# Performance work log

Hardware: AMD Instinct MI355X
Metric: run time of the kernel (lower is better)

## Reference

```python
import jax, jax.numpy as jnp
import numpy as np

NUM_HEADS = 8
CHANNELS = 512


def setup_inputs() -> dict:
    key = jax.random.key(0)
    k1, k2, k3, k4, k5 = jax.random.split(key, 5)
    C = CHANNELS
    x = jax.random.normal(k1, (8, C, 64, 64), dtype=jnp.float32)
    # 1x1 conv weights stored as (out_ch, in_ch) matrices
    qkv_w = jax.random.normal(k2, (3 * C, C), dtype=jnp.float32) * (C ** -0.5)
    qkv_b = jax.random.normal(k3, (3 * C,), dtype=jnp.float32) * 0.02
    proj_w = jax.random.normal(k4, (C, C), dtype=jnp.float32) * (C ** -0.5)
    proj_b = jax.random.normal(k5, (C,), dtype=jnp.float32) * 0.02
    return {"x": x, "qkv_w": qkv_w, "qkv_b": qkv_b, "proj_w": proj_w, "proj_b": proj_b}


def reference(x, qkv_w, qkv_b, proj_w, proj_b):
    B, C, H, W = x.shape
    heads = NUM_HEADS
    d = C // heads
    N = H * W
    scale = d ** -0.5
    # 1x1 conv == per-pixel matmul over channels
    qkv = jnp.einsum('bchw,oc->bohw', x, qkv_w) + qkv_b[None, :, None, None]
    qkv = qkv.reshape(B, 3, heads, d, N)
    q, k, v = qkv[:, 0], qkv[:, 1], qkv[:, 2]  # each (B, heads, d, N)
    # NOTE: attention over the channel dim -> (B, heads, d, d), as in the torch code
    attn = jax.nn.softmax(jnp.einsum('bhdn,bhen->bhde', q, k) * scale, axis=-1)
    # dropout is identity in eval mode
    out = jnp.einsum('bhde,bhen->bhdn', attn, v).reshape(B, C, H, W)
    out = jnp.einsum('bchw,oc->bohw', out, proj_w) + proj_b[None, :, None, None]
    return out, attn.mean(axis=1)  # (B,C,H,W), (B,d,d)
```

## Files before the change

kernel.cpp:

```cpp
#include <hip/hip_runtime.h>
#include <cstdio>
#include <cstdint>

#define BATCH 8
#define CH    512
#define OC3   1536
#define QKROWS 1024
#define NPIX  4096
#define HEADS 8
#define HDIM  64
#define KDEPTH 512
#define SCALE 0.125f
#define NSPLIT 8

typedef __bf16 bf16;
typedef __bf16 bf16x4 __attribute__((ext_vector_type(4)));
typedef __bf16 bf16x8 __attribute__((ext_vector_type(8)));
typedef float  f32x4  __attribute__((ext_vector_type(4)));

#define AS1 __attribute__((address_space(1)))
#define AS3 __attribute__((address_space(3)))

__global__ __launch_bounds__(256) void convert_bf16_kernel(
    const float* __restrict__ in, bf16* __restrict__ out, int n)
{
    const int i = blockIdx.x * 256 + threadIdx.x;
    if (i < n) out[i] = (bf16)in[i];
}

__global__ __launch_bounds__(256) void wvt_kernel(
    const bf16* __restrict__ wv, bf16* __restrict__ wvt)
{
    const int c0 = blockIdx.x * 64;
    const int d0 = blockIdx.y * 64;
    __shared__ bf16 tl[64][72];
    const int t = threadIdx.x;

    #pragma unroll
    for (int i = 0; i < 2; ++i) {
        const int lin = t + 256 * i;
        const int row = lin >> 3;
        const int c8  = (lin & 7) * 8;
        *(bf16x8*)&tl[row][c8] = *(const bf16x8*)(wv + (size_t)(d0 + row) * CH + c0 + c8);
    }
    __syncthreads();
    #pragma unroll
    for (int i = 0; i < 2; ++i) {
        const int lin  = t + 256 * i;
        const int crow = lin >> 3;
        const int d8   = (lin & 7) * 8;
        bf16x8 v;
        #pragma unroll
        for (int j = 0; j < 8; ++j) v[j] = tl[d8 + j][crow];
        *(bf16x8*)(wvt + (size_t)(c0 + crow) * CH + d0 + d8) = v;
    }
}

__global__ __launch_bounds__(256) void transpose_convert_kernel(
    const float* __restrict__ src, bf16* __restrict__ dst)
{
    const int b  = blockIdx.z;
    const int n0 = blockIdx.x * 64;
    const int c0 = blockIdx.y * 64;
    __shared__ float tile[64][65];
    const int t = threadIdx.x;
    const float* xp = src + (size_t)b * CH * NPIX;

    #pragma unroll
    for (int i = 0; i < 4; ++i) {
        const int lin = t + 256 * i;
        const int r   = lin >> 4;
        const int c4  = (lin & 15) * 4;
        const float4 v = *(const float4*)(xp + (size_t)(c0 + r) * 4096 + n0 + c4);
        tile[r][c4 + 0] = v.x; tile[r][c4 + 1] = v.y;
        tile[r][c4 + 2] = v.z; tile[r][c4 + 3] = v.w;
    }
    __syncthreads();

    bf16* op = dst + (size_t)b * NPIX * CH;
    #pragma unroll
    for (int i = 0; i < 2; ++i) {
        const int lin = t + 256 * i;
        const int n   = lin >> 3;
        const int c8  = (lin & 7) * 8;
        bf16x8 v;
        #pragma unroll
        for (int jj = 0; jj < 8; ++jj) v[jj] = (bf16)tile[c8 + jj][n];
        *(bf16x8*)(op + (size_t)(n0 + n) * CH + c0 + c8) = v;
    }
}

__global__ __launch_bounds__(256) void gemm_qk_kernel(
    const bf16* __restrict__ A, const bf16* __restrict__ Bt,
    const float* __restrict__ bias, bf16* __restrict__ qkb)
{
    const int nwg  = gridDim.x * gridDim.y;
    const int orig = blockIdx.x + gridDim.x * blockIdx.y;
    const int wg   = (orig & 7) * (nwg >> 3) + (orig >> 3);
    const int by   = wg % gridDim.y;
    const int bx   = wg / gridDim.y;

    const int b  = blockIdx.z;
    const int m0 = by * 128;
    const int n0 = bx * 128;
    const bf16* Ap = A;
    const bf16* Bp = Bt + (size_t)b * NPIX * KDEPTH;

    __shared__ bf16 smem[16384];

    const int t    = threadIdx.x;
    const int lane = t & 63;
    const int wave = t >> 6;
    const int wr   = wave >> 1, wc = wave & 1;

    f32x4 acc[4][4];
    const f32x4 zf = {0.f, 0.f, 0.f, 0.f};
    #pragma unroll
    for (int i = 0; i < 4; ++i)
        #pragma unroll
        for (int j = 0; j < 4; ++j) acc[i][j] = zf;

    auto STAGE = [&](int p, int k0) {
        #pragma unroll
        for (int i = 0; i < 2; ++i) {
            const int c   = t + 256 * i;
            const int row = c >> 2;
            const int kb  = ((c & 3) ^ ((row >> 1) & 3)) * 8;
            __builtin_amdgcn_global_load_lds(
                (const AS1 void*)(Ap + (size_t)(m0 + row) * KDEPTH + k0 + kb),
                (AS3 void*)(smem + p * 8192 + c * 8), 16, 0, 0);
            __builtin_amdgcn_global_load_lds(
                (const AS1 void*)(Bp + (size_t)(n0 + row) * KDEPTH + k0 + kb),
                (AS3 void*)(smem + p * 8192 + 4096 + c * 8), 16, 0, 0);
        }
    };

    STAGE(0, 0);
    __syncthreads();
    int cur = 0;

    for (int kt = 0; kt < KDEPTH / 32; ++kt) {
        if (kt < KDEPTH / 32 - 1) STAGE(cur ^ 1, (kt + 1) * 32);

        const bf16* AsP = smem + cur * 8192;
        const bf16* BsP = AsP + 4096;
        bf16x8 af[4], bfv[4];
        #pragma unroll
        for (int i = 0; i < 4; ++i) {
            const int ar = wr * 64 + i * 16 + (lane & 15);
            const int ja = (lane >> 4) ^ ((ar >> 1) & 3);
            af[i]  = *(const bf16x8*)(AsP + ar * 32 + ja * 8);
            const int br = wc * 64 + i * 16 + (lane & 15);
            const int jb = (lane >> 4) ^ ((br >> 1) & 3);
            bfv[i] = *(const bf16x8*)(BsP + br * 32 + jb * 8);
        }
        #pragma unroll
        for (int i = 0; i < 4; ++i)
            #pragma unroll
            for (int j = 0; j < 4; ++j)
                acc[i][j] = __builtin_amdgcn_mfma_f32_16x16x32_bf16(
                    af[i], bfv[j], acc[i][j], 0, 0, 0);

        __syncthreads();
        cur ^= 1;
    }

    {
        bf16* ct = smem;
        #pragma unroll
        for (int i = 0; i < 4; ++i) {
            const int ml = wr * 64 + i * 16 + (lane >> 4) * 4;
            #pragma unroll
            for (int r = 0; r < 4; ++r) {
                const float bv = bias[m0 + ml + r];
                #pragma unroll
                for (int j = 0; j < 4; ++j) {
                    const int n = wc * 64 + j * 16 + (lane & 15);
                    ct[(ml + r) * 128 + n] = (bf16)(acc[i][j][r] + bv);
                }
            }
        }
        __syncthreads();
        bf16* Qp = qkb + (size_t)b * QKROWS * NPIX;
        #pragma unroll
        for (int ii = 0; ii < 8; ++ii) {
            const int c   = t + 256 * ii;
            const int row = c >> 4;
            const int seg = c & 15;
            const int4 v = *(const int4*)(ct + row * 128 + seg * 8);
            *(int4*)(Qp + (size_t)(m0 + row) * NPIX + n0 + seg * 8) = v;
        }
    }
}

__global__ __launch_bounds__(256) void qk_partial_kernel(
    const bf16* __restrict__ qk, float* __restrict__ part)
{
    const int s  = blockIdx.x;
    const int bh = blockIdx.y;
    const int b = bh >> 3, h = bh & 7;
    const bf16* qbase = qk + ((size_t)b * QKROWS + h * HDIM) * NPIX;
    const bf16* kbase = qk + ((size_t)b * QKROWS + CH + h * HDIM) * NPIX;

    __shared__ bf16 smem[16384];

    const int t    = threadIdx.x;
    const int lane = t & 63;
    const int wave = t >> 6;

    f32x4 acc[4];
    const f32x4 zf = {0.f, 0.f, 0.f, 0.f};
    #pragma unroll
    for (int j = 0; j < 4; ++j) acc[j] = zf;

    auto STAGE = [&](int p, int n0) {
        #pragma unroll
        for (int i = 0; i < 2; ++i) {
            const int c   = t + 256 * i;
            const int row = c >> 3;
            const int nb  = ((c & 7) ^ (row & 7)) * 8;
            __builtin_amdgcn_global_load_lds(
                (const AS1 void*)(qbase + (size_t)row * NPIX + n0 + nb),
                (AS3 void*)(smem + p * 8192 + c * 8), 16, 0, 0);
            __builtin_amdgcn_global_load_lds(
                (const AS1 void*)(kbase + (size_t)row * NPIX + n0 + nb),
                (AS3 void*)(smem + p * 8192 + 4096 + c * 8), 16, 0, 0);
        }
    };

    STAGE(0, s * 512);
    __syncthreads();
    int cur = 0;

    for (int nc = 0; nc < 8; ++nc) {
        if (nc < 7) STAGE(cur ^ 1, s * 512 + (nc + 1) * 64);

        const bf16* Qs = smem + cur * 8192;
        const bf16* Ks = Qs + 4096;
        #pragma unroll
        for (int ks = 0; ks < 2; ++ks) {
            const int dr = wave * 16 + (lane & 15);
            const int ja = (ks * 4 + (lane >> 4)) ^ (dr & 7);
            const bf16x8 af = *(const bf16x8*)(Qs + dr * 64 + ja * 8);
            #pragma unroll
            for (int j = 0; j < 4; ++j) {
                const int er = j * 16 + (lane & 15);
                const int jb = (ks * 4 + (lane >> 4)) ^ (er & 7);
                const bf16x8 bf_ = *(const bf16x8*)(Ks + er * 64 + jb * 8);
                acc[j] = __builtin_amdgcn_mfma_f32_16x16x32_bf16(af, bf_, acc[j], 0, 0, 0);
            }
        }
        __syncthreads();
        cur ^= 1;
    }

    float* pb = part + (((size_t)bh * NSPLIT + s) * 64) * 64;
    #pragma unroll
    for (int j = 0; j < 4; ++j)
        #pragma unroll
        for (int r = 0; r < 4; ++r)
            pb[(size_t)(wave * 16 + (lane >> 4) * 4 + r) * 64 + j * 16 + (lane & 15)] = acc[j][r];
}

__global__ __launch_bounds__(256) void qk_reduce_softmax_kernel(
    const float* __restrict__ part, float* __restrict__ attn)
{
    const int bh = blockIdx.x;
    const int t  = threadIdx.x;
    const int r  = t >> 2;
    const int e0 = (t & 3) * 16;

    float v[16];
    #pragma unroll
    for (int i = 0; i < 16; ++i) v[i] = 0.f;

    const float* pb = part + ((size_t)bh * NSPLIT * 64) * 64 + r * 64 + e0;
    for (int s = 0; s < NSPLIT; ++s) {
        const float* ps = pb + (size_t)s * 4096;
        #pragma unroll
        for (int c4 = 0; c4 < 4; ++c4) {
            const float4 p = *(const float4*)(ps + c4 * 4);
            v[c4 * 4 + 0] += p.x; v[c4 * 4 + 1] += p.y;
            v[c4 * 4 + 2] += p.z; v[c4 * 4 + 3] += p.w;
        }
    }

    float m = -1e30f;
    #pragma unroll
    for (int i = 0; i < 16; ++i) m = fmaxf(m, v[i]);
    m = fmaxf(m, __shfl_xor(m, 1));
    m = fmaxf(m, __shfl_xor(m, 2));

    float sum = 0.f;
    #pragma unroll
    for (int i = 0; i < 16; ++i) {
        v[i] = __expf((v[i] - m) * SCALE);
        sum += v[i];
    }
    sum += __shfl_xor(sum, 1);
    sum += __shfl_xor(sum, 2);
    const float inv = 1.f / sum;

    float* arow = attn + ((size_t)bh * 64 + r) * 64 + e0;
    #pragma unroll
    for (int c4 = 0; c4 < 4; ++c4) {
        float4 o;
        o.x = v[c4 * 4 + 0] * inv; o.y = v[c4 * 4 + 1] * inv;
        o.z = v[c4 * 4 + 2] * inv; o.w = v[c4 * 4 + 3] * inv;
        *(float4*)(arow + c4 * 4) = o;
    }
}

__global__ __launch_bounds__(256) void attn_mean_kernel(
    const float* __restrict__ attn, float* __restrict__ om)
{
    const int idx = blockIdx.x * 256 + threadIdx.x;
    const int b = idx >> 12, de = idx & 4095;
    float s = 0.f;
    #pragma unroll
    for (int h = 0; h < 8; ++h)
        s += attn[(((size_t)b * 8 + h) << 12) + de];
    om[idx] = s * 0.125f;
}

__global__ __launch_bounds__(256) void wprime_kernel(
    const float* __restrict__ proj_w, const float* __restrict__ attn,
    bf16* __restrict__ wp)
{
    const int o0 = blockIdx.x * 64;
    const int h  = blockIdx.y;
    const int b  = blockIdx.z;

    __shared__ float ws[64][65];
    __shared__ float as_[64][65];

    const int t = threadIdx.x;
    #pragma unroll
    for (int i = 0; i < 4; ++i) {
        const int lin = t + 256 * i;
        const int r   = lin >> 4;
        const int c4  = (lin & 15) * 4;
        const float4 wv = *(const float4*)(proj_w + (size_t)(o0 + r) * CH + h * HDIM + c4);
        ws[r][c4 + 0] = wv.x; ws[r][c4 + 1] = wv.y;
        ws[r][c4 + 2] = wv.z; ws[r][c4 + 3] = wv.w;
        const float4 av = *(const float4*)(attn + (((size_t)(b * 8 + h) * 64) + r) * 64 + c4);
        as_[r][c4 + 0] = av.x; as_[r][c4 + 1] = av.y;
        as_[r][c4 + 2] = av.z; as_[r][c4 + 3] = av.w;
    }
    __syncthreads();

    const int tx = t & 15, ty = t >> 4;
    const int to = ty * 4, te = tx * 4;
    float acc[4][4] = {};
    for (int d = 0; d < 64; ++d) {
        float a[4], bb[4];
        #pragma unroll
        for (int i = 0; i < 4; ++i) a[i]  = ws[to + i][d];
        #pragma unroll
        for (int j = 0; j < 4; ++j) bb[j] = as_[d][te + j];
        #pragma unroll
        for (int i = 0; i < 4; ++i)
            #pragma unroll
            for (int j = 0; j < 4; ++j)
                acc[i][j] = fmaf(a[i], bb[j], acc[i][j]);
    }

    bf16* wb = wp + (size_t)b * CH * CH;
    #pragma unroll
    for (int i = 0; i < 4; ++i)
        #pragma unroll
        for (int j = 0; j < 4; ++j)
            wb[(size_t)(o0 + to + i) * CH + h * HDIM + te + j] = (bf16)acc[i][j];
}

__global__ __launch_bounds__(256) void bias2_kernel(
    const bf16* __restrict__ wp, const float* __restrict__ bv,
    const float* __restrict__ pb, float* __restrict__ bias2)
{
    const int idx = blockIdx.x * 256 + threadIdx.x;
    const int b = idx >> 9, o = idx & 511;
    const bf16* wr = wp + ((size_t)b * CH + o) * CH;
    float s = 0.f;
    for (int d = 0; d < 512; ++d) s += (float)wr[d] * bv[d];
    bias2[idx] = s + pb[o];
}

__global__ __launch_bounds__(256) void gemm128_kernel(
    const bf16* __restrict__ A, const bf16* __restrict__ Bt,
    const float* __restrict__ bias, size_t bias_bstride,
    float* __restrict__ Cf, bf16* __restrict__ Cb,
    int ncols, int c_rows, size_t a_bstride, size_t bt_bstride)
{
    const int nwg  = gridDim.x * gridDim.y;
    const int orig = blockIdx.x + gridDim.x * blockIdx.y;
    const int wg   = (orig & 7) * (nwg >> 3) + (orig >> 3);
    const int by   = wg % gridDim.y;
    const int bx   = wg / gridDim.y;

    const int b  = blockIdx.z;
    const int m0 = by * 128;
    const int n0 = bx * 128;
    const bf16* Ap = A  + (size_t)b * a_bstride;
    const bf16* Bp = Bt + (size_t)b * bt_bstride;

    __shared__ bf16 smem[16384];

    const int t    = threadIdx.x;
    const int lane = t & 63;
    const int wave = t >> 6;
    const int wr   = wave >> 1, wc = wave & 1;

    f32x4 acc[4][4];
    const f32x4 zf = {0.f, 0.f, 0.f, 0.f};
    #pragma unroll
    for (int i = 0; i < 4; ++i)
        #pragma unroll
        for (int j = 0; j < 4; ++j) acc[i][j] = zf;

    auto STAGE = [&](int p, int k0) {
        #pragma unroll
        for (int i = 0; i < 2; ++i) {
            const int c   = t + 256 * i;
            const int row = c >> 2;
            const int kb  = ((c & 3) ^ ((row >> 1) & 3)) * 8;
            __builtin_amdgcn_global_load_lds(
                (const AS1 void*)(Ap + (size_t)(m0 + row) * KDEPTH + k0 + kb),
                (AS3 void*)(smem + p * 8192 + c * 8), 16, 0, 0);
            __builtin_amdgcn_global_load_lds(
                (const AS1 void*)(Bp + (size_t)(n0 + row) * KDEPTH + k0 + kb),
                (AS3 void*)(smem + p * 8192 + 4096 + c * 8), 16, 0, 0);
        }
    };

    STAGE(0, 0);
    __syncthreads();
    int cur = 0;

    for (int kt = 0; kt < KDEPTH / 32; ++kt) {
        if (kt < KDEPTH / 32 - 1) STAGE(cur ^ 1, (kt + 1) * 32);

        const bf16* AsP = smem + cur * 8192;
        const bf16* BsP = AsP + 4096;
        bf16x8 af[4], bfv[4];
        #pragma unroll
        for (int i = 0; i < 4; ++i) {
            const int ar = wr * 64 + i * 16 + (lane & 15);
            const int ja = (lane >> 4) ^ ((ar >> 1) & 3);
            af[i]  = *(const bf16x8*)(AsP + ar * 32 + ja * 8);
            const int br = wc * 64 + i * 16 + (lane & 15);
            const int jb = (lane >> 4) ^ ((br >> 1) & 3);
            bfv[i] = *(const bf16x8*)(BsP + br * 32 + jb * 8);
        }
        #pragma unroll
        for (int i = 0; i < 4; ++i)
            #pragma unroll
            for (int j = 0; j < 4; ++j)
                acc[i][j] = __builtin_amdgcn_mfma_f32_16x16x32_bf16(
                    af[i], bfv[j], acc[i][j], 0, 0, 0);

        __syncthreads();
        cur ^= 1;
    }

    if (Cb) {
        #pragma unroll
        for (int i = 0; i < 4; ++i) {
            const int mb = m0 + wr * 64 + i * 16 + (lane >> 4) * 4;
            #pragma unroll
            for (int r = 0; r < 4; ++r) {
                const int m  = mb + r;
                const float bv = bias ? bias[b * bias_bstride + m] : 0.f;
                #pragma unroll
                for (int j = 0; j < 4; ++j) {
                    const int n = n0 + wc * 64 + j * 16 + (lane & 15);
                    Cb[(size_t)b * c_rows * ncols + (size_t)m * ncols + n] =
                        (bf16)(acc[i][j][r] + bv);
                }
            }
        }
    } else {
        float* ct = (float*)smem;
        float* Cp = Cf + (size_t)b * c_rows * ncols;
        #pragma unroll
        for (int p = 0; p < 2; ++p) {
            if (wc == p) {
                #pragma unroll
                for (int i = 0; i < 4; ++i) {
                    const int ml = wr * 64 + i * 16 + (lane >> 4) * 4;
                    #pragma unroll
                    for (int r = 0; r < 4; ++r) {
                        const float bv = bias ? bias[b * bias_bstride + m0 + ml + r] : 0.f;
                        #pragma unroll
                        for (int j = 0; j < 4; ++j) {
                            const int n = j * 16 + (lane & 15);
                            ct[(ml + r) * 64 + n] = acc[i][j][r] + bv;
                        }
                    }
                }
            }
            __syncthreads();
            #pragma unroll
            for (int ii = 0; ii < 8; ++ii) {
                const int c   = t + 256 * ii;
                const int row = c >> 4;
                const int seg = c & 15;
                const float4 v = *(const float4*)(ct + row * 64 + seg * 4);
                *(float4*)(Cp + (size_t)(m0 + row) * ncols + n0 + p * 64 + seg * 4) = v;
            }
            __syncthreads();
        }
    }
}

extern "C" void kernel_launch(void* const* d_in, const int* in_sizes, int n_in,
                              void* d_out, int out_size, void* d_ws, size_t ws_size,
                              hipStream_t stream)
{
    (void)in_sizes; (void)n_in; (void)out_size;
    const float* x      = (const float*)d_in[0];
    const float* qkv_w  = (const float*)d_in[1];
    const float* qkv_b  = (const float*)d_in[2];
    const float* proj_w = (const float*)d_in[3];
    const float* proj_b = (const float*)d_in[4];

    float* out       = (float*)d_out;
    float* attn_mean = out + (size_t)BATCH * CH * NPIX;

    const size_t qk_bytes   = (size_t)BATCH * QKROWS * NPIX * 2;
    const size_t xt_bytes   = (size_t)BATCH * NPIX * CH * 2;
    const size_t wq_bytes   = (size_t)OC3 * KDEPTH * 2;
    const size_t attn_bytes = (size_t)BATCH * HEADS * HDIM * HDIM * 4;
    const size_t part_bytes = (size_t)BATCH * HEADS * NSPLIT * HDIM * HDIM * 4;
    const size_t wp_bytes   = (size_t)BATCH * CH * CH * 2;
    const size_t wpp_bytes  = (size_t)BATCH * CH * CH * 2;
    const size_t wvt_bytes  = (size_t)CH * CH * 2;
    const size_t b2_bytes   = (size_t)BATCH * CH * 4;
    const size_t need = qk_bytes + xt_bytes + wq_bytes + attn_bytes + part_bytes +
                        wp_bytes + wpp_bytes + wvt_bytes + b2_bytes;
    if (ws_size < need) {
        fprintf(stderr, "[kernel_launch] ws_size=%zu < need=%zu — abort\n", ws_size, need);
        fflush(stderr);
        return;
    }

    char* p = (char*)d_ws;
    bf16*  qk     = (bf16*)p;             p += qk_bytes;
    bf16*  xt     = (bf16*)p;             p += xt_bytes;
    bf16*  wq_b   = (bf16*)p;             p += wq_bytes;
    float* attn   = (float*)p;            p += attn_bytes;
    float* part   = (float*)p;            p += part_bytes;
    bf16*  wprime = (bf16*)p;             p += wp_bytes;
    bf16*  wpp    = (bf16*)p;             p += wpp_bytes;
    bf16*  wvt    = (bf16*)p;             p += wvt_bytes;
    float* bias2  = (float*)p;

    convert_bf16_kernel<<<dim3((OC3 * KDEPTH + 255) / 256), 256, 0, stream>>>(
        qkv_w, wq_b, OC3 * KDEPTH);
    wvt_kernel<<<dim3(8, 8), 256, 0, stream>>>(wq_b + (size_t)2 * CH * KDEPTH, wvt);

    transpose_convert_kernel<<<dim3(NPIX / 64, CH / 64, BATCH), 256, 0, stream>>>(x, xt);

    gemm_qk_kernel<<<dim3(NPIX / 128, QKROWS / 128, BATCH), 256, 0, stream>>>(
        wq_b, xt, qkv_b, qk);

    qk_partial_kernel<<<dim3(NSPLIT, BATCH * HEADS), 256, 0, stream>>>(qk, part);
    qk_reduce_softmax_kernel<<<dim3(BATCH * HEADS), 256, 0, stream>>>(part, attn);

    attn_mean_kernel<<<dim3(BATCH * HDIM * HDIM / 256), 256, 0, stream>>>(attn, attn_mean);

    wprime_kernel<<<dim3(CH / 64, HEADS, BATCH), 256, 0, stream>>>(proj_w, attn, wprime);

    gemm128_kernel<<<dim3(CH / 128, CH / 128, BATCH), 256, 0, stream>>>(
        wprime, wvt, nullptr, 0, nullptr, wpp, CH, CH, (size_t)CH * CH, 0);
    bias2_kernel<<<dim3(BATCH * CH / 256), 256, 0, stream>>>(
        wprime, qkv_b + 2 * CH, proj_b, bias2);

    gemm128_kernel<<<dim3(NPIX / 128, CH / 128, BATCH), 256, 0, stream>>>(
        wpp, xt, bias2, CH, out, nullptr, NPIX, CH, (size_t)CH * CH,
        (size_t)NPIX * KDEPTH);
}
```

Baseline: 162.4 us.

## Triple-buffer GEMM K-loop with raw barriers and fuse weight convert/transpose

Both 128x128 bf16 GEMM kernels move from a double-buffered LDS pipeline to a three-stage ring. Two tiles stay in flight, and a single s_waitcnt vmcnt(4) plus s_barrier per iteration replaces the full __syncthreads. MFMA blocks are wrapped in s_setprio to favour matrix issue, and the weight fp32->bf16 conversion and V-weight transpose are merged into one launch. This aims to hide global-load latency and cut a launch, at the cost of 50% more LDS per block, which may lower occupancy.

```diff
diff --git a/kernel.cpp b/kernel.cpp
--- a/kernel.cpp
+++ b/kernel.cpp
@@ -21,27 +21,30 @@
 #define AS1 __attribute__((address_space(1)))
 #define AS3 __attribute__((address_space(3)))
 
-__global__ __launch_bounds__(256) void convert_bf16_kernel(
-    const float* __restrict__ in, bf16* __restrict__ out, int n)
-{
-    const int i = blockIdx.x * 256 + threadIdx.x;
-    if (i < n) out[i] = (bf16)in[i];
-}
-
-__global__ __launch_bounds__(256) void wvt_kernel(
-    const bf16* __restrict__ wv, bf16* __restrict__ wvt)
-{
-    const int c0 = blockIdx.x * 64;
-    const int d0 = blockIdx.y * 64;
-    __shared__ bf16 tl[64][72];
+__global__ __launch_bounds__(256) void convert_wvt_kernel(
+    const float* __restrict__ qkv_w, bf16* __restrict__ wq_b,
+    bf16* __restrict__ wvt)
+{
+    const int bid = blockIdx.x;
     const int t = threadIdx.x;
-
-    #pragma unroll
-    for (int i = 0; i < 2; ++i) {
+    if (bid < (OC3 * KDEPTH) / 256) {
+        const int i = bid * 256 + t;
+        wq_b[i] = (bf16)qkv_w[i];
+        return;
+    }
+    const int tb = bid - (OC3 * KDEPTH) / 256;
+    const int c0 = (tb & 7) * 64;
+    const int d0 = (tb >> 3) * 64;
+    __shared__ float tl[64][68];
+    const float* wv = qkv_w + (size_t)2 * CH * KDEPTH;
+    #pragma unroll
+    for (int i = 0; i < 4; ++i) {
         const int lin = t + 256 * i;
-        const int row = lin >> 3;
-        const int c8  = (lin & 7) * 8;
-        *(bf16x8*)&tl[row][c8] = *(const bf16x8*)(wv + (size_t)(d0 + row) * CH + c0 + c8);
+        const int row = lin >> 4;
+        const int c4  = (lin & 15) * 4;
+        const float4 v = *(const float4*)(wv + (size_t)(d0 + row) * CH + c0 + c4);
+        tl[row][c4 + 0] = v.x; tl[row][c4 + 1] = v.y;
+        tl[row][c4 + 2] = v.z; tl[row][c4 + 3] = v.w;
     }
     __syncthreads();
     #pragma unroll
@@ -51,7 +54,7 @@
         const int d8   = (lin & 7) * 8;
         bf16x8 v;
         #pragma unroll
-        for (int j = 0; j < 8; ++j) v[j] = tl[d8 + j][crow];
+        for (int j = 0; j < 8; ++j) v[j] = (bf16)tl[d8 + j][crow];
         *(bf16x8*)(wvt + (size_t)(c0 + crow) * CH + d0 + d8) = v;
     }
 }
@@ -106,7 +109,7 @@
     const bf16* Ap = A;
     const bf16* Bp = Bt + (size_t)b * NPIX * KDEPTH;
 
-    __shared__ bf16 smem[16384];
+    __shared__ bf16 smem[3 * 8192];
 
     const int t    = threadIdx.x;
     const int lane = t & 63;
@@ -120,7 +123,9 @@
         #pragma unroll
         for (int j = 0; j < 4; ++j) acc[i][j] = zf;
 
-    auto STAGE = [&](int p, int k0) {
+    auto STAGE = [&](int tile) {
+        bf16* buf = smem + (tile % 3) * 8192;
+        const int k0 = tile * 32;
         #pragma unroll
         for (int i = 0; i < 2; ++i) {
             const int c   = t + 256 * i;
@@ -128,21 +133,15 @@
             const int kb  = ((c & 3) ^ ((row >> 1) & 3)) * 8;
             __builtin_amdgcn_global_load_lds(
                 (const AS1 void*)(Ap + (size_t)(m0 + row) * KDEPTH + k0 + kb),
-                (AS3 void*)(smem + p * 8192 + c * 8), 16, 0, 0);
+                (AS3 void*)(buf + c * 8), 16, 0, 0);
             __builtin_amdgcn_global_load_lds(
                 (const AS1 void*)(Bp + (size_t)(n0 + row) * KDEPTH + k0 + kb),
-                (AS3 void*)(smem + p * 8192 + 4096 + c * 8), 16, 0, 0);
+                (AS3 void*)(buf + 4096 + c * 8), 16, 0, 0);
         }
     };
 
-    STAGE(0, 0);
-    __syncthreads();
-    int cur = 0;
-
-    for (int kt = 0; kt < KDEPTH / 32; ++kt) {
-        if (kt < KDEPTH / 32 - 1) STAGE(cur ^ 1, (kt + 1) * 32);
-
-        const bf16* AsP = smem + cur * 8192;
+    auto COMPUTE = [&](int bufi) {
+        const bf16* AsP = smem + bufi * 8192;
         const bf16* BsP = AsP + 4096;
         bf16x8 af[4], bfv[4];
         #pragma unroll
@@ -154,16 +153,36 @@
             const int jb = (lane >> 4) ^ ((br >> 1) & 3);
             bfv[i] = *(const bf16x8*)(BsP + br * 32 + jb * 8);
         }
+        __builtin_amdgcn_s_setprio(1);
         #pragma unroll
         for (int i = 0; i < 4; ++i)
             #pragma unroll
             for (int j = 0; j < 4; ++j)
                 acc[i][j] = __builtin_amdgcn_mfma_f32_16x16x32_bf16(
                     af[i], bfv[j], acc[i][j], 0, 0, 0);
-
-        __syncthreads();
-        cur ^= 1;
-    }
+        __builtin_amdgcn_s_setprio(0);
+    };
+
+    STAGE(0); STAGE(1);
+    asm volatile("s_waitcnt vmcnt(4)" ::: "memory");
+    asm volatile("s_barrier" ::: "memory");
+
+    int cur = 0;
+    for (int kt = 0; kt < 14; ++kt) {
+        STAGE(kt + 2);
+        COMPUTE(cur);
+        __builtin_amdgcn_sched_barrier(0);
+        asm volatile("s_waitcnt vmcnt(4)" ::: "memory");
+        asm volatile("s_barrier" ::: "memory");
+        cur = (cur + 1) % 3;
+    }
+    COMPUTE(cur);
+    __builtin_amdgcn_sched_barrier(0);
+    asm volatile("s_waitcnt vmcnt(0)" ::: "memory");
+    asm volatile("s_barrier" ::: "memory");
+    cur = (cur + 1) % 3;
+    COMPUTE(cur);
+    __syncthreads();
 
     {
         bf16* ct = smem;
@@ -403,7 +422,7 @@
     const bf16* Ap = A  + (size_t)b * a_bstride;
     const bf16* Bp = Bt + (size_t)b * bt_bstride;
 
-    __shared__ bf16 smem[16384];
+    __shared__ bf16 smem[3 * 8192];
 
     const int t    = threadIdx.x;
     const int lane = t & 63;
@@ -417,7 +436,9 @@
         #pragma unroll
         for (int j = 0; j < 4; ++j) acc[i][j] = zf;
 
-    auto STAGE = [&](int p, int k0) {
+    auto STAGE = [&](int tile) {
+        bf16* buf = smem + (tile % 3) * 8192;
+        const int k0 = tile * 32;
         #pragma unroll
         for (int i = 0; i < 2; ++i) {
             const int c   = t + 256 * i;
@@ -425,21 +446,15 @@
             const int kb  = ((c & 3) ^ ((row >> 1) & 3)) * 8;
             __builtin_amdgcn_global_load_lds(
                 (const AS1 void*)(Ap + (size_t)(m0 + row) * KDEPTH + k0 + kb),
-                (AS3 void*)(smem + p * 8192 + c * 8), 16, 0, 0);
+                (AS3 void*)(buf + c * 8), 16, 0, 0);
             __builtin_amdgcn_global_load_lds(
                 (const AS1 void*)(Bp + (size_t)(n0 + row) * KDEPTH + k0 + kb),
-                (AS3 void*)(smem + p * 8192 + 4096 + c * 8), 16, 0, 0);
+                (AS3 void*)(buf + 4096 + c * 8), 16, 0, 0);
         }
     };
 
-    STAGE(0, 0);
-    __syncthreads();
-    int cur = 0;
-
-    for (int kt = 0; kt < KDEPTH / 32; ++kt) {
-        if (kt < KDEPTH / 32 - 1) STAGE(cur ^ 1, (kt + 1) * 32);
-
-        const bf16* AsP = smem + cur * 8192;
+    auto COMPUTE = [&](int bufi) {
+        const bf16* AsP = smem + bufi * 8192;
         const bf16* BsP = AsP + 4096;
         bf16x8 af[4], bfv[4];
         #pragma unroll
@@ -451,16 +466,36 @@
             const int jb = (lane >> 4) ^ ((br >> 1) & 3);
             bfv[i] = *(const bf16x8*)(BsP + br * 32 + jb * 8);
         }
+        __builtin_amdgcn_s_setprio(1);
         #pragma unroll
         for (int i = 0; i < 4; ++i)
             #pragma unroll
             for (int j = 0; j < 4; ++j)
                 acc[i][j] = __builtin_amdgcn_mfma_f32_16x16x32_bf16(
                     af[i], bfv[j], acc[i][j], 0, 0, 0);
-
-        __syncthreads();
-        cur ^= 1;
-    }
+        __builtin_amdgcn_s_setprio(0);
+    };
+
+    STAGE(0); STAGE(1);
+    asm volatile("s_waitcnt vmcnt(4)" ::: "memory");
+    asm volatile("s_barrier" ::: "memory");
+
+    int cur = 0;
+    for (int kt = 0; kt < 14; ++kt) {
+        STAGE(kt + 2);
+        COMPUTE(cur);
+        __builtin_amdgcn_sched_barrier(0);
+        asm volatile("s_waitcnt vmcnt(4)" ::: "memory");
+        asm volatile("s_barrier" ::: "memory");
+        cur = (cur + 1) % 3;
+    }
+    COMPUTE(cur);
+    __builtin_amdgcn_sched_barrier(0);
+    asm volatile("s_waitcnt vmcnt(0)" ::: "memory");
+    asm volatile("s_barrier" ::: "memory");
+    cur = (cur + 1) % 3;
+    COMPUTE(cur);
+    __syncthreads();
 
     if (Cb) {
         #pragma unroll
@@ -554,9 +589,8 @@
     bf16*  wvt    = (bf16*)p;             p += wvt_bytes;
     float* bias2  = (float*)p;
 
-    convert_bf16_kernel<<<dim3((OC3 * KDEPTH + 255) / 256), 256, 0, stream>>>(
-        qkv_w, wq_b, OC3 * KDEPTH);
-    wvt_kernel<<<dim3(8, 8), 256, 0, stream>>>(wq_b + (size_t)2 * CH * KDEPTH, wvt);
+    convert_wvt_kernel<<<dim3((OC3 * KDEPTH) / 256 + 64), 256, 0, stream>>>(
+        qkv_w, wq_b, wvt);
 
     transpose_convert_kernel<<<dim3(NPIX / 64, CH / 64, BATCH), 256, 0, stream>>>(x, xt);
 
```

Result: faster. 151.3 us (-6.8%).
